# Kernel tuning notes

Measured on AMD Instinct MI355X. Metric: run time of the kernel, lower is better.

Reference implementation:

```python
import jax, jax.numpy as jnp
import numpy as np

N, E, D, H = 100000, 1000000, 64, 64  # nodes, edges, input_dim, output_dim
EPS = 1e-5


def _lin(k, fi, fo):
    return jax.random.normal(k, (fi, fo), jnp.float32) / np.sqrt(fi)


def setup_inputs() -> dict:
    key = jax.random.key(0)
    ks = jax.random.split(key, 8)
    x = jax.random.normal(ks[0], (N, D), jnp.float32)
    e = jax.random.uniform(ks[1], (E,), jnp.float32)
    edge_index = jax.random.randint(ks[2], (2, E), 0, N, dtype=jnp.int32)
    return {
        "x": x,
        "e": e,
        "edge_index": edge_index,
        "W1": _lin(ks[3], 2 * D, H), "b1": jnp.zeros((H,), jnp.float32),
        "g1": jnp.ones((H,), jnp.float32), "be1": jnp.zeros((H,), jnp.float32),
        "W2": _lin(ks[4], H, H), "b2": jnp.zeros((H,), jnp.float32),
        "g2": jnp.ones((H,), jnp.float32), "be2": jnp.zeros((H,), jnp.float32),
        "W3": _lin(ks[5], H, H), "b3": jnp.zeros((H,), jnp.float32),
    }


def _layer_norm(h, g, b):
    mu = jnp.mean(h, axis=-1, keepdims=True)
    var = jnp.mean(jnp.square(h - mu), axis=-1, keepdims=True)
    return (h - mu) * jax.lax.rsqrt(var + EPS) * g + b


def reference(x, e, edge_index, W1, b1, g1, be1, W2, b2, g2, be2, W3, b3):
    start, end = edge_index[0], edge_index[1]
    we = e[:, None]  # [E,1]
    # edge-weighted gather-multiply-scatter_add, both directions
    mi = jax.ops.segment_sum(we * x[start], end, num_segments=N) \
       + jax.ops.segment_sum(we * x[end], start, num_segments=N)  # [N,D]
    h = jnp.concatenate([mi, x], axis=1)  # [N,2D]
    h = jnp.tanh(_layer_norm(h @ W1 + b1, g1, be1))
    h = jnp.tanh(_layer_norm(h @ W2 + b2, g2, be2))
    return h @ W3 + b3  # [N,H]
```

## Files before the change

kernel.cpp:

```cpp
#include <hip/hip_runtime.h>

typedef unsigned int u32;

#define NMAX 100000
#define EMAX 1000000
#define CAP 96
#define NSHMAX 12500

__device__ __align__(16) float g_mi[NMAX * 64];
__device__ int g_deg[8 * NSHMAX];
__device__ __align__(16) u32 g_adj[(size_t)8 * NSHMAX * CAP];

__global__ __launch_bounds__(256) void zero_deg(int n) {
    int i = blockIdx.x * 256 + threadIdx.x;
    if (i < n) g_deg[i] = 0;
}

__global__ __launch_bounds__(256) void fill_sharded(
    const int* __restrict__ src, const int* __restrict__ dst,
    const float* __restrict__ ew, int E, int NSH, int nchunk)
{
    int group = blockIdx.x & 7;
    int chunk = blockIdx.x >> 3;
    int stride = nchunk * 256;
    for (int e = chunk * 256 + threadIdx.x; e < E; e += stride) {
        int s = src[e], t = dst[e];
        float w = ew[e];
        int w15 = (int)(w * 32768.f + 0.5f);
        if (w15 > 32767) w15 = 32767;
        if ((s & 7) == group) {
            int idx = group * NSH + (s >> 3);
            int p = atomicAdd(&g_deg[idx], 1);
            if (p < CAP) g_adj[(size_t)idx * CAP + p] = ((u32)t << 15) | (u32)w15;
        }
        if ((t & 7) == group) {
            int idx = group * NSH + (t >> 3);
            int q = atomicAdd(&g_deg[idx], 1);
            if (q < CAP) g_adj[(size_t)idx * CAP + q] = ((u32)s << 15) | (u32)w15;
        }
    }
}

__global__ __launch_bounds__(256) void gather(const float* __restrict__ x,
                                              int N, int NSH) {
    int wid = (blockIdx.x * 256 + threadIdx.x) >> 6;
    int lane = threadIdx.x & 63;
    if (wid >= N) return;
    int idx = (wid & 7) * NSH + (wid >> 3);
    int cnt = g_deg[idx];
    if (cnt > CAP) cnt = CAP;
    const u32* row = g_adj + (size_t)idx * CAP;
    float acc = 0.f;

    for (int b = 0; b < cnt; b += 64) {
        int m = cnt - b;
        if (m > 64) m = 64;
        u32 ent = (lane < m) ? row[b + lane] : 0u;
        int nbr = (int)(ent >> 15);
        float wv = (float)(ent & 0x7FFFu) * (1.f / 32768.f);

        int j = 0;
        for (; j + 4 <= m; j += 4) {
            int n0 = __shfl(nbr, j + 0);
            int n1 = __shfl(nbr, j + 1);
            int n2 = __shfl(nbr, j + 2);
            int n3 = __shfl(nbr, j + 3);
            float w0 = __shfl(wv, j + 0);
            float w1 = __shfl(wv, j + 1);
            float w2 = __shfl(wv, j + 2);
            float w3 = __shfl(wv, j + 3);
            float v0 = x[(size_t)n0 * 64 + lane];
            float v1 = x[(size_t)n1 * 64 + lane];
            float v2 = x[(size_t)n2 * 64 + lane];
            float v3 = x[(size_t)n3 * 64 + lane];
            acc = fmaf(w0, v0, acc);
            acc = fmaf(w1, v1, acc);
            acc = fmaf(w2, v2, acc);
            acc = fmaf(w3, v3, acc);
        }
        for (; j < m; j++) {
            int nb = __shfl(nbr, j);
            float w = __shfl(wv, j);
            acc = fmaf(w, x[(size_t)nb * 64 + lane], acc);
        }
    }
    g_mi[(size_t)wid * 64 + lane] = acc;
}

#define HS 65

__global__ __launch_bounds__(256, 4) void mlp(
    const float* __restrict__ x,
    const float* __restrict__ W1, const float* __restrict__ B1,
    const float* __restrict__ G1, const float* __restrict__ E1,
    const float* __restrict__ W2, const float* __restrict__ B2,
    const float* __restrict__ G2, const float* __restrict__ E2,
    const float* __restrict__ W3, const float* __restrict__ B3,
    float* __restrict__ out, int N)
{
    __shared__ float hbuf[128 * HS];
    __shared__ float lnb[4 * 64];

    int tid = threadIdx.x;
    int n0 = blockIdx.x * 128;
    int nodes = N - n0; if (nodes > 128) nodes = 128;

    int tx = tid & 7;
    int ty = tid >> 3;

    if (tid < 64) {
        lnb[tid]       = G1[tid];
        lnb[64 + tid]  = E1[tid];
        lnb[128 + tid] = G2[tid];
        lnb[192 + tid] = E2[tid];
    }

    float acc[4][8];
    {
        float bc[8];
        #pragma unroll
        for (int c = 0; c < 8; c++) bc[c] = B1[tx * 8 + c];
        #pragma unroll
        for (int r = 0; r < 4; r++)
            #pragma unroll
            for (int c = 0; c < 8; c++) acc[r][c] = bc[c];
    }

    for (int i = tid; i < 128 * 16; i += 256) {
        int nd = i >> 4, f4 = (i & 15) * 4;
        float4 v = make_float4(0.f, 0.f, 0.f, 0.f);
        if (nd < nodes) v = *(const float4*)&g_mi[(size_t)(n0 + nd) * 64 + f4];
        hbuf[nd * HS + f4 + 0] = v.x;
        hbuf[nd * HS + f4 + 1] = v.y;
        hbuf[nd * HS + f4 + 2] = v.z;
        hbuf[nd * HS + f4 + 3] = v.w;
    }
    __syncthreads();
    #pragma unroll 4
    for (int k = 0; k < 64; k++) {
        float4 w0 = *(const float4*)&W1[k * 64 + tx * 8];
        float4 w1 = *(const float4*)&W1[k * 64 + tx * 8 + 4];
        float a0 = hbuf[(ty * 4 + 0) * HS + k];
        float a1 = hbuf[(ty * 4 + 1) * HS + k];
        float a2 = hbuf[(ty * 4 + 2) * HS + k];
        float a3 = hbuf[(ty * 4 + 3) * HS + k];
        float w[8] = {w0.x, w0.y, w0.z, w0.w, w1.x, w1.y, w1.z, w1.w};
        float a[4] = {a0, a1, a2, a3};
        #pragma unroll
        for (int r = 0; r < 4; r++)
            #pragma unroll
            for (int c = 0; c < 8; c++)
                acc[r][c] = fmaf(a[r], w[c], acc[r][c]);
    }
    __syncthreads();

    for (int i = tid; i < 128 * 16; i += 256) {
        int nd = i >> 4, f4 = (i & 15) * 4;
        float4 v = make_float4(0.f, 0.f, 0.f, 0.f);
        if (nd < nodes) v = *(const float4*)&x[(size_t)(n0 + nd) * 64 + f4];
        hbuf[nd * HS + f4 + 0] = v.x;
        hbuf[nd * HS + f4 + 1] = v.y;
        hbuf[nd * HS + f4 + 2] = v.z;
        hbuf[nd * HS + f4 + 3] = v.w;
    }
    __syncthreads();
    #pragma unroll 4
    for (int k = 0; k < 64; k++) {
        float4 w0 = *(const float4*)&W1[(64 + k) * 64 + tx * 8];
        float4 w1 = *(const float4*)&W1[(64 + k) * 64 + tx * 8 + 4];
        float a0 = hbuf[(ty * 4 + 0) * HS + k];
        float a1 = hbuf[(ty * 4 + 1) * HS + k];
        float a2 = hbuf[(ty * 4 + 2) * HS + k];
        float a3 = hbuf[(ty * 4 + 3) * HS + k];
        float w[8] = {w0.x, w0.y, w0.z, w0.w, w1.x, w1.y, w1.z, w1.w};
        float a[4] = {a0, a1, a2, a3};
        #pragma unroll
        for (int r = 0; r < 4; r++)
            #pragma unroll
            for (int c = 0; c < 8; c++)
                acc[r][c] = fmaf(a[r], w[c], acc[r][c]);
    }
    __syncthreads();
    #pragma unroll
    for (int r = 0; r < 4; r++)
        #pragma unroll
        for (int c = 0; c < 8; c++)
            hbuf[(ty * 4 + r) * HS + tx * 8 + c] = acc[r][c];
    __syncthreads();

    if (tid < 128) {
        float mu = 0.f;
        for (int j = 0; j < 64; j++) mu += hbuf[tid * HS + j];
        mu *= (1.f / 64.f);
        float var = 0.f;
        for (int j = 0; j < 64; j++) { float d = hbuf[tid * HS + j] - mu; var += d * d; }
        var *= (1.f / 64.f);
        float rs = rsqrtf(var + 1e-5f);
        for (int j = 0; j < 64; j++) {
            float v = (hbuf[tid * HS + j] - mu) * rs * lnb[j] + lnb[64 + j];
            float ex = __expf(2.f * v);
            hbuf[tid * HS + j] = 1.f - 2.f / (ex + 1.f);
        }
    }
    __syncthreads();

    {
        float bc[8];
        #pragma unroll
        for (int c = 0; c < 8; c++) bc[c] = B2[tx * 8 + c];
        #pragma unroll
        for (int r = 0; r < 4; r++)
            #pragma unroll
            for (int c = 0; c < 8; c++) acc[r][c] = bc[c];
    }
    #pragma unroll 4
    for (int k = 0; k < 64; k++) {
        float4 w0 = *(const float4*)&W2[k * 64 + tx * 8];
        float4 w1 = *(const float4*)&W2[k * 64 + tx * 8 + 4];
        float a0 = hbuf[(ty * 4 + 0) * HS + k];
        float a1 = hbuf[(ty * 4 + 1) * HS + k];
        float a2 = hbuf[(ty * 4 + 2) * HS + k];
        float a3 = hbuf[(ty * 4 + 3) * HS + k];
        float w[8] = {w0.x, w0.y, w0.z, w0.w, w1.x, w1.y, w1.z, w1.w};
        float a[4] = {a0, a1, a2, a3};
        #pragma unroll
        for (int r = 0; r < 4; r++)
            #pragma unroll
            for (int c = 0; c < 8; c++)
                acc[r][c] = fmaf(a[r], w[c], acc[r][c]);
    }
    __syncthreads();
    #pragma unroll
    for (int r = 0; r < 4; r++)
        #pragma unroll
        for (int c = 0; c < 8; c++)
            hbuf[(ty * 4 + r) * HS + tx * 8 + c] = acc[r][c];
    __syncthreads();

    if (tid < 128) {
        float mu = 0.f;
        for (int j = 0; j < 64; j++) mu += hbuf[tid * HS + j];
        mu *= (1.f / 64.f);
        float var = 0.f;
        for (int j = 0; j < 64; j++) { float d = hbuf[tid * HS + j] - mu; var += d * d; }
        var *= (1.f / 64.f);
        float rs = rsqrtf(var + 1e-5f);
        for (int j = 0; j < 64; j++) {
            float v = (hbuf[tid * HS + j] - mu) * rs * lnb[128 + j] + lnb[192 + j];
            float ex = __expf(2.f * v);
            hbuf[tid * HS + j] = 1.f - 2.f / (ex + 1.f);
        }
    }
    __syncthreads();

    {
        float bc[8];
        #pragma unroll
        for (int c = 0; c < 8; c++) bc[c] = B3[tx * 8 + c];
        #pragma unroll
        for (int r = 0; r < 4; r++)
            #pragma unroll
            for (int c = 0; c < 8; c++) acc[r][c] = bc[c];
    }
    #pragma unroll 4
    for (int k = 0; k < 64; k++) {
        float4 w0 = *(const float4*)&W3[k * 64 + tx * 8];
        float4 w1 = *(const float4*)&W3[k * 64 + tx * 8 + 4];
        float a0 = hbuf[(ty * 4 + 0) * HS + k];
        float a1 = hbuf[(ty * 4 + 1) * HS + k];
        float a2 = hbuf[(ty * 4 + 2) * HS + k];
        float a3 = hbuf[(ty * 4 + 3) * HS + k];
        float w[8] = {w0.x, w0.y, w0.z, w0.w, w1.x, w1.y, w1.z, w1.w};
        float a[4] = {a0, a1, a2, a3};
        #pragma unroll
        for (int r = 0; r < 4; r++)
            #pragma unroll
            for (int c = 0; c < 8; c++)
                acc[r][c] = fmaf(a[r], w[c], acc[r][c]);
    }
    #pragma unroll
    for (int r = 0; r < 4; r++) {
        int nd = ty * 4 + r;
        if (nd < nodes) {
            float* po = out + (size_t)(n0 + nd) * 64 + tx * 8;
            *(float4*)(po)     = make_float4(acc[r][0], acc[r][1], acc[r][2], acc[r][3]);
            *(float4*)(po + 4) = make_float4(acc[r][4], acc[r][5], acc[r][6], acc[r][7]);
        }
    }
}

extern "C" void kernel_launch(void* const* d_in, const int* in_sizes, int n_in,
                              void* d_out, int out_size, void* d_ws, size_t ws_size,
                              hipStream_t stream) {
    const float* x  = (const float*)d_in[0];
    const float* e  = (const float*)d_in[1];
    const int* ei   = (const int*)d_in[2];
    const float* W1 = (const float*)d_in[3];
    const float* b1 = (const float*)d_in[4];
    const float* g1 = (const float*)d_in[5];
    const float* be1= (const float*)d_in[6];
    const float* W2 = (const float*)d_in[7];
    const float* b2 = (const float*)d_in[8];
    const float* g2 = (const float*)d_in[9];
    const float* be2= (const float*)d_in[10];
    const float* W3 = (const float*)d_in[11];
    const float* b3 = (const float*)d_in[12];

    int N = in_sizes[0] / 64;
    int E = in_sizes[1];
    int NSH = (N + 7) / 8;
    int ndeg = 8 * NSH;

    zero_deg<<<(ndeg + 255) / 256, 256, 0, stream>>>(ndeg);

    int nchunk = 256;
    fill_sharded<<<8 * nchunk, 256, 0, stream>>>(ei, ei + E, e, E, NSH, nchunk);

    gather<<<(N * 64 + 255) / 256, 256, 0, stream>>>(x, N, NSH);

    mlp<<<(N + 127) / 128, 256, 0, stream>>>(
        x, W1, b1, g1, be1, W2, b2, g2, be2, W3, b3, (float*)d_out, N);
}
```

Baseline: 340.1 us.

## Read edges once in fill with vectorized loads and shrink MLP node tile

Replaces the 8-way sharded fill, which re-read every edge once per shard group, with a single pass where each thread loads 4 edges via vector loads and inserts both directions. The MLP kernel processes 64 nodes per block instead of 128, with a higher occupancy bound. This cuts redundant edge-list reads, but the atomics become more scattered within a wave, and the smaller tile lowers register reuse of the weight loads.

```diff
diff --git a/kernel.cpp b/kernel.cpp
--- a/kernel.cpp
+++ b/kernel.cpp
@@ -16,27 +16,44 @@
     if (i < n) g_deg[i] = 0;
 }
 
-__global__ __launch_bounds__(256) void fill_sharded(
+__global__ __launch_bounds__(256) void fill_once(
     const int* __restrict__ src, const int* __restrict__ dst,
-    const float* __restrict__ ew, int E, int NSH, int nchunk)
+    const float* __restrict__ ew, int E, int NSH)
 {
-    int group = blockIdx.x & 7;
-    int chunk = blockIdx.x >> 3;
-    int stride = nchunk * 256;
-    for (int e = chunk * 256 + threadIdx.x; e < E; e += stride) {
-        int s = src[e], t = dst[e];
-        float w = ew[e];
-        int w15 = (int)(w * 32768.f + 0.5f);
-        if (w15 > 32767) w15 = 32767;
-        if ((s & 7) == group) {
-            int idx = group * NSH + (s >> 3);
-            int p = atomicAdd(&g_deg[idx], 1);
-            if (p < CAP) g_adj[(size_t)idx * CAP + p] = ((u32)t << 15) | (u32)w15;
-        }
-        if ((t & 7) == group) {
-            int idx = group * NSH + (t >> 3);
-            int q = atomicAdd(&g_deg[idx], 1);
-            if (q < CAP) g_adj[(size_t)idx * CAP + q] = ((u32)s << 15) | (u32)w15;
+    int e0 = (blockIdx.x * 256 + threadIdx.x) * 4;
+    if (e0 >= E) return;
+
+    if (e0 + 3 < E) {
+        int4   s4 = *(const int4*)&src[e0];
+        int4   t4 = *(const int4*)&dst[e0];
+        float4 w4 = *(const float4*)&ew[e0];
+        int   sv[4] = {s4.x, s4.y, s4.z, s4.w};
+        int   tv[4] = {t4.x, t4.y, t4.z, t4.w};
+        float wv[4] = {w4.x, w4.y, w4.z, w4.w};
+        #pragma unroll
+        for (int j = 0; j < 4; j++) {
+            int s = sv[j], t = tv[j];
+            int w15 = (int)(wv[j] * 32768.f + 0.5f);
+            if (w15 > 32767) w15 = 32767;
+            int is = (s & 7) * NSH + (s >> 3);
+            int p = atomicAdd(&g_deg[is], 1);
+            if (p < CAP) g_adj[(size_t)is * CAP + p] = ((u32)t << 15) | (u32)w15;
+            int it = (t & 7) * NSH + (t >> 3);
+            int q = atomicAdd(&g_deg[it], 1);
+            if (q < CAP) g_adj[(size_t)it * CAP + q] = ((u32)s << 15) | (u32)w15;
+        }
+    } else {
+        for (int e = e0; e < E; e++) {
+            int s = src[e], t = dst[e];
+            float w = ew[e];
+            int w15 = (int)(w * 32768.f + 0.5f);
+            if (w15 > 32767) w15 = 32767;
+            int is = (s & 7) * NSH + (s >> 3);
+            int p = atomicAdd(&g_deg[is], 1);
+            if (p < CAP) g_adj[(size_t)is * CAP + p] = ((u32)t << 15) | (u32)w15;
+            int it = (t & 7) * NSH + (t >> 3);
+            int q = atomicAdd(&g_deg[it], 1);
+            if (q < CAP) g_adj[(size_t)it * CAP + q] = ((u32)s << 15) | (u32)w15;
         }
     }
 }
@@ -89,7 +106,7 @@
 
 #define HS 65
 
-__global__ __launch_bounds__(256, 4) void mlp(
+__global__ __launch_bounds__(256, 8) void mlp(
     const float* __restrict__ x,
     const float* __restrict__ W1, const float* __restrict__ B1,
     const float* __restrict__ G1, const float* __restrict__ E1,
@@ -98,12 +115,12 @@
     const float* __restrict__ W3, const float* __restrict__ B3,
     float* __restrict__ out, int N)
 {
-    __shared__ float hbuf[128 * HS];
+    __shared__ float hbuf[64 * HS];
     __shared__ float lnb[4 * 64];
 
     int tid = threadIdx.x;
-    int n0 = blockIdx.x * 128;
-    int nodes = N - n0; if (nodes > 128) nodes = 128;
+    int n0 = blockIdx.x * 64;
+    int nodes = N - n0; if (nodes > 64) nodes = 64;
 
     int tx = tid & 7;
     int ty = tid >> 3;
@@ -115,18 +132,18 @@
         lnb[192 + tid] = E2[tid];
     }
 
-    float acc[4][8];
+    float acc[2][8];
     {
         float bc[8];
         #pragma unroll
         for (int c = 0; c < 8; c++) bc[c] = B1[tx * 8 + c];
         #pragma unroll
-        for (int r = 0; r < 4; r++)
+        for (int r = 0; r < 2; r++)
             #pragma unroll
             for (int c = 0; c < 8; c++) acc[r][c] = bc[c];
     }
 
-    for (int i = tid; i < 128 * 16; i += 256) {
+    for (int i = tid; i < 64 * 16; i += 256) {
         int nd = i >> 4, f4 = (i & 15) * 4;
         float4 v = make_float4(0.f, 0.f, 0.f, 0.f);
         if (nd < nodes) v = *(const float4*)&g_mi[(size_t)(n0 + nd) * 64 + f4];
@@ -140,21 +157,19 @@
     for (int k = 0; k < 64; k++) {
         float4 w0 = *(const float4*)&W1[k * 64 + tx * 8];
         float4 w1 = *(const float4*)&W1[k * 64 + tx * 8 + 4];
-        float a0 = hbuf[(ty * 4 + 0) * HS + k];
-        float a1 = hbuf[(ty * 4 + 1) * HS + k];
-        float a2 = hbuf[(ty * 4 + 2) * HS + k];
-        float a3 = hbuf[(ty * 4 + 3) * HS + k];
+        float a0 = hbuf[(ty * 2 + 0) * HS + k];
+        float a1 = hbuf[(ty * 2 + 1) * HS + k];
         float w[8] = {w0.x, w0.y, w0.z, w0.w, w1.x, w1.y, w1.z, w1.w};
-        float a[4] = {a0, a1, a2, a3};
-        #pragma unroll
-        for (int r = 0; r < 4; r++)
+        float a[2] = {a0, a1};
+        #pragma unroll
+        for (int r = 0; r < 2; r++)
             #pragma unroll
             for (int c = 0; c < 8; c++)
                 acc[r][c] = fmaf(a[r], w[c], acc[r][c]);
     }
     __syncthreads();
 
-    for (int i = tid; i < 128 * 16; i += 256) {
+    for (int i = tid; i < 64 * 16; i += 256) {
         int nd = i >> 4, f4 = (i & 15) * 4;
         float4 v = make_float4(0.f, 0.f, 0.f, 0.f);
         if (nd < nodes) v = *(const float4*)&x[(size_t)(n0 + nd) * 64 + f4];
@@ -168,27 +183,25 @@
     for (int k = 0; k < 64; k++) {
         float4 w0 = *(const float4*)&W1[(64 + k) * 64 + tx * 8];
         float4 w1 = *(const float4*)&W1[(64 + k) * 64 + tx * 8 + 4];
-        float a0 = hbuf[(ty * 4 + 0) * HS + k];
-        float a1 = hbuf[(ty * 4 + 1) * HS + k];
-        float a2 = hbuf[(ty * 4 + 2) * HS + k];
-        float a3 = hbuf[(ty * 4 + 3) * HS + k];
+        float a0 = hbuf[(ty * 2 + 0) * HS + k];
+        float a1 = hbuf[(ty * 2 + 1) * HS + k];
         float w[8] = {w0.x, w0.y, w0.z, w0.w, w1.x, w1.y, w1.z, w1.w};
-        float a[4] = {a0, a1, a2, a3};
-        #pragma unroll
-        for (int r = 0; r < 4; r++)
+        float a[2] = {a0, a1};
+        #pragma unroll
+        for (int r = 0; r < 2; r++)
             #pragma unroll
             for (int c = 0; c < 8; c++)
                 acc[r][c] = fmaf(a[r], w[c], acc[r][c]);
     }
     __syncthreads();
     #pragma unroll
-    for (int r = 0; r < 4; r++)
+    for (int r = 0; r < 2; r++)
         #pragma unroll
         for (int c = 0; c < 8; c++)
-            hbuf[(ty * 4 + r) * HS + tx * 8 + c] = acc[r][c];
-    __syncthreads();
-
-    if (tid < 128) {
+            hbuf[(ty * 2 + r) * HS + tx * 8 + c] = acc[r][c];
+    __syncthreads();
+
+    if (tid < 64) {
         float mu = 0.f;
         for (int j = 0; j < 64; j++) mu += hbuf[tid * HS + j];
         mu *= (1.f / 64.f);
@@ -209,7 +222,7 @@
         #pragma unroll
         for (int c = 0; c < 8; c++) bc[c] = B2[tx * 8 + c];
         #pragma unroll
-        for (int r = 0; r < 4; r++)
+        for (int r = 0; r < 2; r++)
             #pragma unroll
             for (int c = 0; c < 8; c++) acc[r][c] = bc[c];
     }
@@ -217,27 +230,25 @@
     for (int k = 0; k < 64; k++) {
         float4 w0 = *(const float4*)&W2[k * 64 + tx * 8];
         float4 w1 = *(const float4*)&W2[k * 64 + tx * 8 + 4];
-        float a0 = hbuf[(ty * 4 + 0) * HS + k];
-        float a1 = hbuf[(ty * 4 + 1) * HS + k];
-        float a2 = hbuf[(ty * 4 + 2) * HS + k];
-        float a3 = hbuf[(ty * 4 + 3) * HS + k];
+        float a0 = hbuf[(ty * 2 + 0) * HS + k];
+        float a1 = hbuf[(ty * 2 + 1) * HS + k];
         float w[8] = {w0.x, w0.y, w0.z, w0.w, w1.x, w1.y, w1.z, w1.w};
-        float a[4] = {a0, a1, a2, a3};
-        #pragma unroll
-        for (int r = 0; r < 4; r++)
+        float a[2] = {a0, a1};
+        #pragma unroll
+        for (int r = 0; r < 2; r++)
             #pragma unroll
             for (int c = 0; c < 8; c++)
                 acc[r][c] = fmaf(a[r], w[c], acc[r][c]);
     }
     __syncthreads();
     #pragma unroll
-    for (int r = 0; r < 4; r++)
+    for (int r = 0; r < 2; r++)
         #pragma unroll
         for (int c = 0; c < 8; c++)
-            hbuf[(ty * 4 + r) * HS + tx * 8 + c] = acc[r][c];
-    __syncthreads();
-
-    if (tid < 128) {
+            hbuf[(ty * 2 + r) * HS + tx * 8 + c] = acc[r][c];
+    __syncthreads();
+
+    if (tid < 64) {
         float mu = 0.f;
         for (int j = 0; j < 64; j++) mu += hbuf[tid * HS + j];
         mu *= (1.f / 64.f);
@@ -258,7 +269,7 @@
         #pragma unroll
         for (int c = 0; c < 8; c++) bc[c] = B3[tx * 8 + c];
         #pragma unroll
-        for (int r = 0; r < 4; r++)
+        for (int r = 0; r < 2; r++)
             #pragma unroll
             for (int c = 0; c < 8; c++) acc[r][c] = bc[c];
     }
@@ -266,21 +277,19 @@
     for (int k = 0; k < 64; k++) {
         float4 w0 = *(const float4*)&W3[k * 64 + tx * 8];
         float4 w1 = *(const float4*)&W3[k * 64 + tx * 8 + 4];
-        float a0 = hbuf[(ty * 4 + 0) * HS + k];
-        float a1 = hbuf[(ty * 4 + 1) * HS + k];
-        float a2 = hbuf[(ty * 4 + 2) * HS + k];
-        float a3 = hbuf[(ty * 4 + 3) * HS + k];
+        float a0 = hbuf[(ty * 2 + 0) * HS + k];
+        float a1 = hbuf[(ty * 2 + 1) * HS + k];
         float w[8] = {w0.x, w0.y, w0.z, w0.w, w1.x, w1.y, w1.z, w1.w};
-        float a[4] = {a0, a1, a2, a3};
-        #pragma unroll
-        for (int r = 0; r < 4; r++)
+        float a[2] = {a0, a1};
+        #pragma unroll
+        for (int r = 0; r < 2; r++)
             #pragma unroll
             for (int c = 0; c < 8; c++)
                 acc[r][c] = fmaf(a[r], w[c], acc[r][c]);
     }
     #pragma unroll
-    for (int r = 0; r < 4; r++) {
-        int nd = ty * 4 + r;
+    for (int r = 0; r < 2; r++) {
+        int nd = ty * 2 + r;
         if (nd < nodes) {
             float* po = out + (size_t)(n0 + nd) * 64 + tx * 8;
             *(float4*)(po)     = make_float4(acc[r][0], acc[r][1], acc[r][2], acc[r][3]);
@@ -313,11 +322,11 @@
 
     zero_deg<<<(ndeg + 255) / 256, 256, 0, stream>>>(ndeg);
 
-    int nchunk = 256;
-    fill_sharded<<<8 * nchunk, 256, 0, stream>>>(ei, ei + E, e, E, NSH, nchunk);
+    int nfb = (E / 4 + 255) / 256;
+    fill_once<<<nfb, 256, 0, stream>>>(ei, ei + E, e, E, NSH);
 
     gather<<<(N * 64 + 255) / 256, 256, 0, stream>>>(x, N, NSH);
 
-    mlp<<<(N + 127) / 128, 256, 0, stream>>>(
+    mlp<<<(N + 63) / 64, 256, 0, stream>>>(
         x, W1, b1, g1, be1, W2, b2, g2, be2, W3, b3, (float*)d_out, N);
 }
```

Measured after the change: 459.4 us. 35.1% more time.
